# Optimization experiments

Measured on AMD Instinct MI355X. Metric: run time of the kernel, lower is better.

The kernel has to match this reference:

```python
import jax, jax.numpy as jnp
import numpy as np

N = 50000   # nodes
E = 800000  # edges (avg degree 16)
D = 128     # in_dim == hidden_dim


def setup_inputs() -> dict:
    key = jax.random.key(0)
    ks = jax.random.split(key, 8)
    x = jax.random.normal(ks[0], (N, D), dtype=jnp.float32)
    edge_index = jax.random.randint(ks[1], (2, E), 0, N, dtype=jnp.int32)
    s = 1.0 / np.sqrt(D)  # glorot-ish scale
    W0 = jax.random.normal(ks[2], (D, D), dtype=jnp.float32) * s
    W1 = jax.random.normal(ks[3], (D, D), dtype=jnp.float32) * s
    W2 = jax.random.normal(ks[4], (D, D), dtype=jnp.float32) * s
    b0 = jnp.zeros((D,), dtype=jnp.float32)
    b1 = jnp.zeros((D,), dtype=jnp.float32)
    b2 = jnp.zeros((D,), dtype=jnp.float32)
    return {"x": x, "edge_index": edge_index,
            "W0": W0, "b0": b0, "W1": W1, "b1": b1, "W2": W2, "b2": b2}


def reference(x, edge_index, W0, b0, W1, b1, W2, b2):
    # PyG GCNConv defaults: add self-loops, symmetric D^-1/2 (A+I) D^-1/2 norm,
    # linear transform first, bias added after aggregation.
    src, dst = edge_index[0], edge_index[1]
    loops = jnp.arange(N, dtype=src.dtype)
    src_f = jnp.concatenate([src, loops])  # [E+N]
    dst_f = jnp.concatenate([dst, loops])
    deg = jax.ops.segment_sum(jnp.ones_like(src_f, dtype=x.dtype), dst_f, num_segments=N)
    dinv = jnp.where(deg > 0, jax.lax.rsqrt(deg), 0.0)
    norm = dinv[src_f] * dinv[dst_f]  # [E+N]

    def gcn_layer(h, W, b):
        h = h @ W                                # [N, D]
        msg = h[src_f] * norm[:, None]           # [E+N, D] gather
        agg = jax.ops.segment_sum(msg, dst_f, num_segments=N)  # scatter-add
        return agg + b

    h = jax.nn.relu(gcn_layer(x, W0, b0))  # dropout p=0.0 is a no-op
    h = jax.nn.relu(gcn_layer(h, W1, b1))
    return gcn_layer(h, W2, b2)
```

## Files before the change

### kernel.cpp

```cpp
#include <hip/hip_runtime.h>
#include <hip/hip_fp16.h>

#define NN 50000
#define NPAD 50048
#define NE 800000
#define D 128
#define BPAD 136
#define EGRID 3125
#define NB 196

typedef __attribute__((ext_vector_type(8))) short bf16x8;
typedef __attribute__((ext_vector_type(4))) float f32x4;

__device__ inline unsigned short f2bf(float f) {
    unsigned int b = __float_as_uint(f);
    return (unsigned short)((b + 0x7FFFu + ((b >> 16) & 1u)) >> 16);
}
__device__ inline float bf2f(unsigned short u) {
    return __uint_as_float(((unsigned int)u) << 16);
}


__global__ void k_degree_convW(const int* __restrict__ dst, int* __restrict__ cnt,
                               int* __restrict__ rank,
                               const float* __restrict__ W0, const float* __restrict__ W1,
                               const float* __restrict__ W2,
                               unsigned short* __restrict__ Wh, unsigned short* __restrict__ Wl) {
    int bid = blockIdx.x;
    int t = threadIdx.x;
    if (bid < EGRID) {
        int e = bid * 256 + t;
        if (e < NE) {
            int d = dst[e];
            int r = atomicAdd(&cnt[d], 1);
            __builtin_nontemporal_store(r, &rank[e]);
        }
    } else {
        int i = (bid - EGRID) * 256 + t;
        if (i >= 3 * D * D) return;
        int m = i / (D * D), r = i - m * (D * D);
        const float* W = (m == 0) ? W0 : ((m == 1) ? W1 : W2);
        int k = r >> 7, c = r & 127;
        float v = W[r];
        unsigned short h = f2bf(v);
        unsigned short l = f2bf(v - bf2f(h));
        Wh[(size_t)m * D * D + c * D + k] = h;
        Wl[(size_t)m * D * D + c * D + k] = l;
    }
}

__global__ void k_scan_block(const int* __restrict__ cnt, int* __restrict__ excl,
                             int* __restrict__ bsum, int* __restrict__ boff,
                             int* __restrict__ counter) {
    __shared__ int sm[256];
    __shared__ int lastflag;
    int t = threadIdx.x;
    int idx = blockIdx.x * 256 + t;
    int v = (idx < NN) ? cnt[idx] : 0;
    sm[t] = v;
    __syncthreads();
    for (int o = 1; o < 256; o <<= 1) {
        int u = (t >= o) ? sm[t - o] : 0;
        __syncthreads();
        sm[t] += u;
        __syncthreads();
    }
    if (idx < NN) excl[idx] = sm[t] - v;
    if (t == 255) bsum[blockIdx.x] = sm[255];
    __threadfence();
    if (t == 0) {
        int ticket = atomicAdd(counter, 1);
        lastflag = (ticket == NB - 1);
    }
    __syncthreads();
    if (!lastflag) return;
    __threadfence();
    int v2 = (t < NB) ? bsum[t] : 0;
    sm[t] = v2;
    __syncthreads();
    for (int o = 1; o < 256; o <<= 1) {
        int u = (t >= o) ? sm[t - o] : 0;
        __syncthreads();
        sm[t] += u;
        __syncthreads();
    }
    if (t < NB) boff[t] = sm[t] - v2;
}

__global__ void k_scan_add(int* __restrict__ rowptr, const int* __restrict__ boff,
                           const int* __restrict__ cnt, float* __restrict__ dinv) {
    int idx = blockIdx.x * 256 + threadIdx.x;
    if (idx < NN) {
        rowptr[idx] += boff[idx >> 8];
        dinv[idx] = rsqrtf((float)(cnt[idx] + 1));
    } else if (idx == NN) {
        rowptr[NN] = NE;
    }
}

__global__ void k_fill(const int* __restrict__ src, const int* __restrict__ dst,
                       const int* __restrict__ rowptr, const int* __restrict__ rank,
                       int* __restrict__ col) {
    int e = blockIdx.x * 256 + threadIdx.x;
    if (e < NE) {
        int d = dst[e];
        int pos = rowptr[d] + rank[e];
        __builtin_nontemporal_store(src[e], &col[pos]);
    }
}


__device__ inline void gemm_store(f32x4 acc[2][4], const float* __restrict__ dinv,
                                  __half* __restrict__ C, int R0, int C0, int lr, int lg) {
    #pragma unroll
    for (int fr = 0; fr < 2; fr++) {
        int rb = R0 + fr * 16 + lg * 4;
        #pragma unroll
        for (int j = 0; j < 4; j++) {
            int r = rb + j;
            if (r < NN) {
                float s = dinv[r];
                #pragma unroll
                for (int fc = 0; fc < 4; fc++)
                    C[(size_t)r * D + C0 + fc * 16 + lr] =
                        __float2half_rn(acc[fr][fc][j] * s);
            }
        }
    }
}


__global__ __launch_bounds__(256, 2) void k_gemm_mfma_x(
        const float* __restrict__ X,
        const unsigned short* __restrict__ BhT, const unsigned short* __restrict__ BlT,
        const float* __restrict__ dinv, __half* __restrict__ C) {
    __shared__ short Bs_h[D * BPAD];
    int t = threadIdx.x;
    {
        int c = t >> 1;
        int k0 = (t & 1) * 64;
        const unsigned short* gh = BhT + c * D + k0;
        short* dh = Bs_h + c * BPAD + k0;
        #pragma unroll
        for (int i = 0; i < 8; i++)
            *(int4*)(dh + i * 8) = *(const int4*)(gh + i * 8);
    }
    __syncthreads();

    int w = t >> 6, ln = t & 63;
    int wr = w >> 1, wc = w & 1;
    int R0 = blockIdx.x * 64 + wr * 32;
    int C0 = wc * 64;
    int lr = ln & 15, lg = ln >> 4;

    f32x4 acc[2][4];
    #pragma unroll
    for (int a = 0; a < 2; a++)
        #pragma unroll
        for (int b = 0; b < 4; b++)
            acc[a][b] = (f32x4){0.f, 0.f, 0.f, 0.f};

    const float* Ab = X + (size_t)(R0 + lr) * D + lg * 8;

    #pragma unroll
    for (int ks = 0; ks < 4; ks++) {
        int ko = ks * 32;
        bf16x8 fa_h[2], fa_l[2], fb_h[4], fb_l[4];
        #pragma unroll
        for (int fr = 0; fr < 2; fr++) {
            float4 p0 = *(const float4*)(Ab + fr * 16 * D + ko);
            float4 p1 = *(const float4*)(Ab + fr * 16 * D + ko + 4);
            float vv[8] = {p0.x, p0.y, p0.z, p0.w, p1.x, p1.y, p1.z, p1.w};
            #pragma unroll
            for (int j = 0; j < 8; j++) {
                unsigned short h = f2bf(vv[j]);
                fa_h[fr][j] = (short)h;
                fa_l[fr][j] = (short)f2bf(vv[j] - bf2f(h));
            }
        }
        #pragma unroll
        for (int fc = 0; fc < 4; fc++) {
            int ccol = C0 + fc * 16 + lr;
            fb_h[fc] = *(const bf16x8*)(Bs_h + ccol * BPAD + ko + lg * 8);
            fb_l[fc] = *(const bf16x8*)(BlT + (size_t)ccol * D + ko + lg * 8);
        }
        #pragma unroll
        for (int fr = 0; fr < 2; fr++) {
            #pragma unroll
            for (int fc = 0; fc < 4; fc++) {
                acc[fr][fc] = __builtin_amdgcn_mfma_f32_16x16x32_bf16(
                    fa_h[fr], fb_h[fc], acc[fr][fc], 0, 0, 0);
                acc[fr][fc] = __builtin_amdgcn_mfma_f32_16x16x32_bf16(
                    fa_l[fr], fb_h[fc], acc[fr][fc], 0, 0, 0);
                acc[fr][fc] = __builtin_amdgcn_mfma_f32_16x16x32_bf16(
                    fa_h[fr], fb_l[fc], acc[fr][fc], 0, 0, 0);
            }
        }
    }
    gemm_store(acc, dinv, C, R0, C0, lr, lg);
}


__global__ __launch_bounds__(256, 3) void k_gemm_mfma_h(
        const __half* __restrict__ H,
        const unsigned short* __restrict__ BhT, const unsigned short* __restrict__ BlT,
        const float* __restrict__ dinv, __half* __restrict__ C) {
    __shared__ short Bs_h[D * BPAD];
    int t = threadIdx.x;
    {
        int c = t >> 1;
        int k0 = (t & 1) * 64;
        const unsigned short* gh = BhT + c * D + k0;
        short* dh = Bs_h + c * BPAD + k0;
        #pragma unroll
        for (int i = 0; i < 8; i++)
            *(int4*)(dh + i * 8) = *(const int4*)(gh + i * 8);
    }
    __syncthreads();

    int w = t >> 6, ln = t & 63;
    int wr = w >> 1, wc = w & 1;
    int R0 = blockIdx.x * 64 + wr * 32;
    int C0 = wc * 64;
    int lr = ln & 15, lg = ln >> 4;

    f32x4 acc[2][4];
    #pragma unroll
    for (int a = 0; a < 2; a++)
        #pragma unroll
        for (int b = 0; b < 4; b++)
            acc[a][b] = (f32x4){0.f, 0.f, 0.f, 0.f};

    const __half* Ab = H + (size_t)(R0 + lr) * D + lg * 8;

    #pragma unroll
    for (int ks = 0; ks < 4; ks++) {
        int ko = ks * 32;
        bf16x8 fa_h[2], fa_l[2], fb_h[4], fb_l[4];
        #pragma unroll
        for (int fr = 0; fr < 2; fr++) {
            float4 p = *(const float4*)(Ab + fr * 16 * D + ko);
            const __half2* hp = (const __half2*)&p;
            #pragma unroll
            for (int q = 0; q < 4; q++) {
                float2 fv = __half22float2(hp[q]);
                unsigned short h0 = f2bf(fv.x), h1 = f2bf(fv.y);
                fa_h[fr][q * 2]     = (short)h0;
                fa_h[fr][q * 2 + 1] = (short)h1;
                fa_l[fr][q * 2]     = (short)f2bf(fv.x - bf2f(h0));
                fa_l[fr][q * 2 + 1] = (short)f2bf(fv.y - bf2f(h1));
            }
        }
        #pragma unroll
        for (int fc = 0; fc < 4; fc++) {
            int ccol = C0 + fc * 16 + lr;
            fb_h[fc] = *(const bf16x8*)(Bs_h + ccol * BPAD + ko + lg * 8);
            fb_l[fc] = *(const bf16x8*)(BlT + (size_t)ccol * D + ko + lg * 8);
        }
        #pragma unroll
        for (int fr = 0; fr < 2; fr++) {
            #pragma unroll
            for (int fc = 0; fc < 4; fc++) {
                acc[fr][fc] = __builtin_amdgcn_mfma_f32_16x16x32_bf16(
                    fa_h[fr], fb_h[fc], acc[fr][fc], 0, 0, 0);
                acc[fr][fc] = __builtin_amdgcn_mfma_f32_16x16x32_bf16(
                    fa_l[fr], fb_h[fc], acc[fr][fc], 0, 0, 0);
                acc[fr][fc] = __builtin_amdgcn_mfma_f32_16x16x32_bf16(
                    fa_h[fr], fb_l[fc], acc[fr][fc], 0, 0, 0);
            }
        }
    }
    gemm_store(acc, dinv, C, R0, C0, lr, lg);
}


__device__ inline void agg_accum(const float4& rv, float a[8]) {
    const __half2* hp = (const __half2*)&rv;
    #pragma unroll
    for (int q = 0; q < 4; q++) {
        float2 fv = __half22float2(hp[q]);
        a[q * 2] += fv.x;
        a[q * 2 + 1] += fv.y;
    }
}

__device__ inline void agg_core(const __half* __restrict__ T,
                                const int* __restrict__ rowptr,
                                const int* __restrict__ col,
                                int i, int f, int lane, float a[8]) {
    int gb = lane & 48;
    int sl8 = lane & 7;
    {
        float4 raw = *(const float4*)(T + (size_t)i * D + f);
        const __half2* hp = (const __half2*)&raw;
        #pragma unroll
        for (int q = 0; q < 4; q++) {
            float2 fv = __half22float2(hp[q]);
            a[q * 2] = fv.x;
            a[q * 2 + 1] = fv.y;
        }
    }
    int r0 = rowptr[i], r1 = rowptr[i + 1];
    for (int e = r0; e < r1; e += 8) {
        int idx = e + sl8;
        if (idx > r1 - 1) idx = r1 - 1;
        int cv = col[idx];
        int m = r1 - e;
        m = m > 8 ? 8 : m;
        int ss[8];
        #pragma unroll
        for (int u = 0; u < 8; u++) ss[u] = __shfl(cv, gb + u, 64);
        float4 rv[8];
        #pragma unroll
        for (int u = 0; u < 8; u++)
            rv[u] = *(const float4*)(T + (size_t)ss[u] * D + f);
        #pragma unroll
        for (int u = 0; u < 8; u++)
            if (u < m) agg_accum(rv[u], a);
    }
}

__global__ __launch_bounds__(256) void k_agg_relu(const __half* __restrict__ T,
                                                  const int* __restrict__ rowptr,
                                                  const int* __restrict__ col,
                                                  const float* __restrict__ dinv,
                                                  const float* __restrict__ bias,
                                                  __half* __restrict__ Hout) {
    int i = blockIdx.x * 16 + (threadIdx.x >> 4);
    int lane = threadIdx.x & 63;
    int sl = threadIdx.x & 15;
    int f = sl * 8;
    float di = dinv[i];
    float a[8];
    agg_core(T, rowptr, col, i, f, lane, a);
    float4 bv0 = *(const float4*)(bias + f);
    float4 bv1 = *(const float4*)(bias + f + 4);
    float bb[8] = {bv0.x, bv0.y, bv0.z, bv0.w, bv1.x, bv1.y, bv1.z, bv1.w};
    __half2 o[4];
    #pragma unroll
    for (int q = 0; q < 4; q++) {
        float x0 = fmaxf(a[q * 2] * di + bb[q * 2], 0.f);
        float x1 = fmaxf(a[q * 2 + 1] * di + bb[q * 2 + 1], 0.f);
        o[q] = __floats2half2_rn(x0, x1);
    }
    *(float4*)(Hout + (size_t)i * D + f) = *(float4*)o;
}

__global__ __launch_bounds__(256) void k_agg_out(const __half* __restrict__ T,
                                                 const int* __restrict__ rowptr,
                                                 const int* __restrict__ col,
                                                 const float* __restrict__ dinv,
                                                 const float* __restrict__ bias,
                                                 float* __restrict__ Of) {
    int i = blockIdx.x * 16 + (threadIdx.x >> 4);
    int lane = threadIdx.x & 63;
    int sl = threadIdx.x & 15;
    int f = sl * 8;
    float di = dinv[i];
    float a[8];
    agg_core(T, rowptr, col, i, f, lane, a);
    float4 bv0 = *(const float4*)(bias + f);
    float4 bv1 = *(const float4*)(bias + f + 4);
    float4 o0 = make_float4(a[0] * di + bv0.x, a[1] * di + bv0.y,
                            a[2] * di + bv0.z, a[3] * di + bv0.w);
    float4 o1 = make_float4(a[4] * di + bv1.x, a[5] * di + bv1.y,
                            a[6] * di + bv1.z, a[7] * di + bv1.w);
    *(float4*)(Of + (size_t)i * D + f) = o0;
    *(float4*)(Of + (size_t)i * D + f + 4) = o1;
}


extern "C" void kernel_launch(void* const* d_in, const int* in_sizes, int n_in,
                              void* d_out, int out_size, void* d_ws, size_t ws_size,
                              hipStream_t stream) {
    const float* x  = (const float*)d_in[0];
    const int* edge = (const int*)d_in[1];
    const float* W0 = (const float*)d_in[2];
    const float* b0 = (const float*)d_in[3];
    const float* W1 = (const float*)d_in[4];
    const float* b1 = (const float*)d_in[5];
    const float* W2 = (const float*)d_in[6];
    const float* b2 = (const float*)d_in[7];
    const int* src = edge;
    const int* dst = edge + NE;
    float* out = (float*)d_out;

    char* ws = (char*)d_ws;
    size_t off = 0;
    auto alloc = [&](size_t bytes) {
        void* p = ws + off;
        off += (bytes + 255) & ~(size_t)255;
        return p;
    };
    int*   cnt     = (int*)alloc(NN * 4);
    int*   counter = (int*)alloc(256);
    int*   rowptr  = (int*)alloc((NN + 1) * 4);
    float* dinv    = (float*)alloc(NN * 4);
    int*   bsum    = (int*)alloc(256 * 4);
    int*   boff    = (int*)alloc(256 * 4);
    int*   rank    = (int*)alloc((size_t)NE * 4);
    int*   col     = (int*)alloc((size_t)NE * 4);
    unsigned short* Wh = (unsigned short*)alloc(3 * D * D * 2);
    unsigned short* Wl = (unsigned short*)alloc(3 * D * D * 2);
    __half* Ta = (__half*)alloc((size_t)NPAD * D * 2);
    __half* Tb = (__half*)alloc((size_t)NPAD * D * 2);
    __half* Hb = (__half*)alloc((size_t)NPAD * D * 2);

    hipMemsetAsync(cnt, 0, NN * 4, stream);
    hipMemsetAsync(counter, 0, 256, stream);

    k_degree_convW<<<EGRID + 192, 256, 0, stream>>>(dst, cnt, rank, W0, W1, W2, Wh, Wl);
    k_scan_block<<<NB, 256, 0, stream>>>(cnt, rowptr, bsum, boff, counter);
    k_scan_add<<<(NN + 256) / 256, 256, 0, stream>>>(rowptr, boff, cnt, dinv);
    k_fill<<<EGRID, 256, 0, stream>>>(src, dst, rowptr, rank, col);

    const int ggrid = (NN + 63) / 64;
    const int agrid = NN / 16;

    k_gemm_mfma_x<<<ggrid, 256, 0, stream>>>(x, Wh, Wl, dinv, Ta);
    k_agg_relu<<<agrid, 256, 0, stream>>>(Ta, rowptr, col, dinv, b0, Hb);
    k_gemm_mfma_h<<<ggrid, 256, 0, stream>>>(Hb, Wh + D * D, Wl + D * D, dinv, Tb);
    k_agg_relu<<<agrid, 256, 0, stream>>>(Tb, rowptr, col, dinv, b1, Hb);
    k_gemm_mfma_h<<<ggrid, 256, 0, stream>>>(Hb, Wh + 2 * D * D, Wl + 2 * D * D, dinv, Ta);
    k_agg_out<<<agrid, 256, 0, stream>>>(Ta, rowptr, col, dinv, b2, out);
}
```

Measured before the change: 238.5 us.

## Assign four lanes per node in aggregation, looping over feature quarters

Each node in the aggregation kernels is now handled by 4 lanes instead of 16. Each lane walks the node's neighbour list four times, covering a 32-feature slice per pass, and the grid shrinks to 64 nodes per block. The aim is to spread edge-loop divergence from uneven degrees across more nodes per wavefront and to raise the number of in-flight gathers per lane. The cost is four reloads of the column indices and narrower 64-byte row segments per gather, which may hurt memory coalescing.

```diff
diff --git a/kernel.cpp b/kernel.cpp
--- a/kernel.cpp
+++ b/kernel.cpp
@@ -284,12 +284,10 @@
     }
 }
 
-__device__ inline void agg_core(const __half* __restrict__ T,
-                                const int* __restrict__ rowptr,
+__device__ inline void agg_pass(const __half* __restrict__ T,
                                 const int* __restrict__ col,
-                                int i, int f, int lane, float a[8]) {
-    int gb = lane & 48;
-    int sl8 = lane & 7;
+                                int r0, int r1, int i, int f, int gb, int sl4,
+                                float a[8]) {
     {
         float4 raw = *(const float4*)(T + (size_t)i * D + f);
         const __half2* hp = (const __half2*)&raw;
@@ -300,16 +298,17 @@
             a[q * 2 + 1] = fv.y;
         }
     }
-    int r0 = rowptr[i], r1 = rowptr[i + 1];
     for (int e = r0; e < r1; e += 8) {
-        int idx = e + sl8;
-        if (idx > r1 - 1) idx = r1 - 1;
-        int cv = col[idx];
-        int m = r1 - e;
-        m = m > 8 ? 8 : m;
+        int i0 = e + sl4;     if (i0 > r1 - 1) i0 = r1 - 1;
+        int i1 = e + 4 + sl4; if (i1 > r1 - 1) i1 = r1 - 1;
+        int c0 = col[i0];
+        int c1 = col[i1];
+        int m = r1 - e; m = m > 8 ? 8 : m;
         int ss[8];
         #pragma unroll
-        for (int u = 0; u < 8; u++) ss[u] = __shfl(cv, gb + u, 64);
+        for (int u = 0; u < 4; u++) ss[u] = __shfl(c0, gb + u, 64);
+        #pragma unroll
+        for (int u = 0; u < 4; u++) ss[4 + u] = __shfl(c1, gb + u, 64);
         float4 rv[8];
         #pragma unroll
         for (int u = 0; u < 8; u++)
@@ -326,24 +325,29 @@
                                                   const float* __restrict__ dinv,
                                                   const float* __restrict__ bias,
                                                   __half* __restrict__ Hout) {
-    int i = blockIdx.x * 16 + (threadIdx.x >> 4);
+    int i = blockIdx.x * 64 + (threadIdx.x >> 2);
+    if (i >= NN) return;
     int lane = threadIdx.x & 63;
-    int sl = threadIdx.x & 15;
-    int f = sl * 8;
+    int gb = lane & 60, sl4 = lane & 3;
     float di = dinv[i];
-    float a[8];
-    agg_core(T, rowptr, col, i, f, lane, a);
-    float4 bv0 = *(const float4*)(bias + f);
-    float4 bv1 = *(const float4*)(bias + f + 4);
-    float bb[8] = {bv0.x, bv0.y, bv0.z, bv0.w, bv1.x, bv1.y, bv1.z, bv1.w};
-    __half2 o[4];
-    #pragma unroll
+    int r0 = rowptr[i], r1 = rowptr[i + 1];
+    #pragma unroll 1
     for (int q = 0; q < 4; q++) {
-        float x0 = fmaxf(a[q * 2] * di + bb[q * 2], 0.f);
-        float x1 = fmaxf(a[q * 2 + 1] * di + bb[q * 2 + 1], 0.f);
-        o[q] = __floats2half2_rn(x0, x1);
-    }
-    *(float4*)(Hout + (size_t)i * D + f) = *(float4*)o;
+        int f = q * 32 + sl4 * 8;
+        float a[8];
+        agg_pass(T, col, r0, r1, i, f, gb, sl4, a);
+        float4 bv0 = *(const float4*)(bias + f);
+        float4 bv1 = *(const float4*)(bias + f + 4);
+        float bb[8] = {bv0.x, bv0.y, bv0.z, bv0.w, bv1.x, bv1.y, bv1.z, bv1.w};
+        __half2 o[4];
+        #pragma unroll
+        for (int p = 0; p < 4; p++) {
+            float x0 = fmaxf(a[p * 2] * di + bb[p * 2], 0.f);
+            float x1 = fmaxf(a[p * 2 + 1] * di + bb[p * 2 + 1], 0.f);
+            o[p] = __floats2half2_rn(x0, x1);
+        }
+        *(float4*)(Hout + (size_t)i * D + f) = *(float4*)o;
+    }
 }
 
 __global__ __launch_bounds__(256) void k_agg_out(const __half* __restrict__ T,
@@ -352,21 +356,26 @@
                                                  const float* __restrict__ dinv,
                                                  const float* __restrict__ bias,
                                                  float* __restrict__ Of) {
-    int i = blockIdx.x * 16 + (threadIdx.x >> 4);
+    int i = blockIdx.x * 64 + (threadIdx.x >> 2);
+    if (i >= NN) return;
     int lane = threadIdx.x & 63;
-    int sl = threadIdx.x & 15;
-    int f = sl * 8;
+    int gb = lane & 60, sl4 = lane & 3;
     float di = dinv[i];
-    float a[8];
-    agg_core(T, rowptr, col, i, f, lane, a);
-    float4 bv0 = *(const float4*)(bias + f);
-    float4 bv1 = *(const float4*)(bias + f + 4);
-    float4 o0 = make_float4(a[0] * di + bv0.x, a[1] * di + bv0.y,
-                            a[2] * di + bv0.z, a[3] * di + bv0.w);
-    float4 o1 = make_float4(a[4] * di + bv1.x, a[5] * di + bv1.y,
-                            a[6] * di + bv1.z, a[7] * di + bv1.w);
-    *(float4*)(Of + (size_t)i * D + f) = o0;
-    *(float4*)(Of + (size_t)i * D + f + 4) = o1;
+    int r0 = rowptr[i], r1 = rowptr[i + 1];
+    #pragma unroll 1
+    for (int q = 0; q < 4; q++) {
+        int f = q * 32 + sl4 * 8;
+        float a[8];
+        agg_pass(T, col, r0, r1, i, f, gb, sl4, a);
+        float4 bv0 = *(const float4*)(bias + f);
+        float4 bv1 = *(const float4*)(bias + f + 4);
+        float4 o0 = make_float4(a[0] * di + bv0.x, a[1] * di + bv0.y,
+                                a[2] * di + bv0.z, a[3] * di + bv0.w);
+        float4 o1 = make_float4(a[4] * di + bv1.x, a[5] * di + bv1.y,
+                                a[6] * di + bv1.z, a[7] * di + bv1.w);
+        *(float4*)(Of + (size_t)i * D + f) = o0;
+        *(float4*)(Of + (size_t)i * D + f + 4) = o1;
+    }
 }
 
 
@@ -415,7 +424,7 @@
     k_fill<<<EGRID, 256, 0, stream>>>(src, dst, rowptr, rank, col);
 
     const int ggrid = (NN + 63) / 64;
-    const int agrid = NN / 16;
+    const int agrid = (NN + 63) / 64;
 
     k_gemm_mfma_x<<<ggrid, 256, 0, stream>>>(x, Wh, Wl, dinv, Ta);
     k_agg_relu<<<agrid, 256, 0, stream>>>(Ta, rowptr, col, dinv, b0, Hb);
```

Result: slower. 285.9 us (+19.8%).
